# Optimization experiments

Hardware: AMD Instinct MI355X
Metric: run time of the kernel (lower is better)

The kernel has to match this reference:

```python
import jax, jax.numpy as jnp
import numpy as np
import itertools

B, H, W, C = 64, 28, 28, 576
NH, WS = 18, 7
KD = C // NH          # head dim = 32 (attn_ratio=1 so d == key_dim)
HID = 4 * C           # mlp hidden
N = WS * WS           # tokens per window = 49


def _bias_idxs():
    points = list(itertools.product(range(WS), range(WS)))
    offsets, idxs = {}, []
    for p1 in points:
        for p2 in points:
            off = (abs(p1[0] - p2[0]), abs(p1[1] - p2[1]))
            if off not in offsets:
                offsets[off] = len(offsets)
            idxs.append(offsets[off])
    return np.asarray(idxs, dtype=np.int64).reshape(N, N), len(offsets)


def setup_inputs() -> dict:
    key = jax.random.key(0)
    ks = jax.random.split(key, 10)
    idxs, n_off = _bias_idxs()  # n_off == 49
    s = 0.02
    return {
        "x": jax.random.normal(ks[0], (B, H * W, C), jnp.float32),
        "gamma_a": jnp.ones((C,), jnp.float32),
        "beta_a": jnp.zeros((C,), jnp.float32),
        "qkv_w": jax.random.normal(ks[1], (3 * C, C), jnp.float32) * s,
        "qkv_b": jnp.zeros((3 * C,), jnp.float32),
        "proj_w": jax.random.normal(ks[2], (C, C), jnp.float32) * s,
        "proj_b": jnp.zeros((C,), jnp.float32),
        "attn_biases": jax.random.normal(ks[3], (NH, n_off), jnp.float32) * s,
        "conv_w": jax.random.normal(ks[4], (C, 1, 3, 3), jnp.float32) * 0.1,
        "bn_gamma": jnp.ones((C,), jnp.float32),
        "bn_beta": jnp.zeros((C,), jnp.float32),
        "bn_mean": jnp.zeros((C,), jnp.float32),
        "bn_var": jax.random.uniform(ks[5], (C,), jnp.float32, 0.5, 1.5),
        "gamma_m": jnp.ones((C,), jnp.float32),
        "beta_m": jnp.zeros((C,), jnp.float32),
        "fc1_w": jax.random.normal(ks[6], (HID, C), jnp.float32) * s,
        "fc1_b": jnp.zeros((HID,), jnp.float32),
        "fc2_w": jax.random.normal(ks[7], (C, HID), jnp.float32) * s,
        "fc2_b": jnp.zeros((C,), jnp.float32),
        "bias_idxs": jnp.asarray(idxs),
    }


def _ln(x, g, b, eps=1e-5):
    mu = x.mean(-1, keepdims=True)
    var = ((x - mu) ** 2).mean(-1, keepdims=True)
    return (x - mu) * jax.lax.rsqrt(var + eps) * g + b


def reference(x, gamma_a, beta_a, qkv_w, qkv_b, proj_w, proj_b, attn_biases,
              conv_w, bn_gamma, bn_beta, bn_mean, bn_var,
              gamma_m, beta_m, fc1_w, fc1_b, fc2_w, fc2_b, bias_idxs):
    scale = KD ** -0.5
    nWh, nWw = H // WS, W // WS
    res = x
    # ---- window partition: (B, H*W, C) -> (B*nWh*nWw, 49, C) ----
    xw = x.reshape(B, nWh, WS, nWw, WS, C).transpose(0, 1, 3, 2, 4, 5)
    xw = xw.reshape(-1, N, C)
    # ---- windowed attention with gathered relative-position bias ----
    h = _ln(xw, gamma_a, beta_a)
    qkv = h @ qkv_w.T + qkv_b                       # (Bw, N, 3C)
    qkv = qkv.reshape(-1, N, NH, 3 * KD)
    q, k, v = jnp.split(qkv, 3, axis=-1)            # each (Bw, N, NH, KD)
    q = q.transpose(0, 2, 1, 3)
    k = k.transpose(0, 2, 1, 3)
    v = v.transpose(0, 2, 1, 3)
    bias = attn_biases[:, bias_idxs]                # (NH, N, N)
    attn = jnp.einsum('bhnd,bhmd->bhnm', q, k) * scale + bias
    attn = jax.nn.softmax(attn, axis=-1)
    out = jnp.einsum('bhnm,bhmd->bhnd', attn, v)    # (Bw, NH, N, KD)
    out = out.transpose(0, 2, 1, 3).reshape(-1, N, C) @ proj_w.T + proj_b
    # ---- window reverse ----
    out = out.reshape(B, nWh, nWw, WS, WS, C).transpose(0, 1, 3, 2, 4, 5)
    out = out.reshape(B, H * W, C)
    x = res + out
    # ---- depthwise 3x3 conv + BatchNorm (inference stats) ----
    xc = x.transpose(0, 2, 1).reshape(B, C, H, W)
    xc = jax.lax.conv_general_dilated(
        xc, conv_w, (1, 1), [(1, 1), (1, 1)],
        feature_group_count=C,
        dimension_numbers=('NCHW', 'OIHW', 'NCHW'))
    eps = 1e-5
    inv = (jax.lax.rsqrt(bn_var + eps) * bn_gamma)[:, None, None]
    xc = (xc - bn_mean[:, None, None]) * inv + bn_beta[:, None, None]
    x = xc.reshape(B, C, H * W).transpose(0, 2, 1)
    # ---- MLP with pre-LayerNorm ----
    hm = _ln(x, gamma_m, beta_m)
    hm = jax.nn.gelu(hm @ fc1_w.T + fc1_b, approximate=False)
    hm = hm @ fc2_w.T + fc2_b
    return x + hm
```

## Files before the change

kernel.cpp:

```cpp
#include <hip/hip_runtime.h>
#include <hip/hip_bf16.h>

typedef __bf16 v8bf  __attribute__((ext_vector_type(8)));
typedef __bf16 v4bf  __attribute__((ext_vector_type(4)));
typedef float  f32x4 __attribute__((ext_vector_type(4)));
typedef float  f32x8 __attribute__((ext_vector_type(8)));

#define TOKENS 50176
#define CDIM   576
#define NHEAD  18
#define QKVD   1728

__device__ __forceinline__ void gld16(const __bf16* g, __bf16* l)
{
    __builtin_amdgcn_global_load_lds(
        (const __attribute__((address_space(1))) void*)g,
        (__attribute__((address_space(3))) void*)l,
        16, 0, 0);
}

__device__ __forceinline__ float fast_gelu(float x)
{
    const float z  = x * 0.70710678118654752f;
    const float az = fabsf(z);
    const float t  = __frcp_rn(1.0f + 0.3275911f * az);
    float p = 1.061405429f;
    p = p * t - 1.453152027f;
    p = p * t + 1.421413741f;
    p = p * t - 0.284496736f;
    p = p * t + 0.254829592f;
    const float e   = __expf(-z * z);
    float erfv = 1.0f - p * t * e;
    erfv = copysignf(erfv, z);
    return 0.5f * x * (1.0f + erfv);
}

__global__ __launch_bounds__(256)
void cast4_kernel(const float* __restrict__ s0, const float* __restrict__ s1,
                  const float* __restrict__ s2, const float* __restrict__ s3,
                  __bf16* __restrict__ dst)
{
    const size_t i = ((size_t)blockIdx.x * 256 + threadIdx.x) * 4;
    constexpr size_t n0 = (size_t)QKVD * CDIM;
    constexpr size_t n1 = n0 + (size_t)CDIM * CDIM;
    constexpr size_t n2 = n1 + (size_t)2304 * CDIM;
    const float* s; size_t off;
    if (i < n0)      { s = s0; off = i; }
    else if (i < n1) { s = s1; off = i - n0; }
    else if (i < n2) { s = s2; off = i - n1; }
    else             { s = s3; off = i - n2; }
    f32x4 v = *(const f32x4*)&s[off];
    v4bf o;
#pragma unroll
    for (int j = 0; j < 4; ++j) o[j] = (__bf16)v[j];
    *(v4bf*)&dst[i] = o;
}

__global__ __launch_bounds__(64)
void conv_prep(const float* __restrict__ w, const float* __restrict__ bg,
               const float* __restrict__ bb, const float* __restrict__ bm,
               const float* __restrict__ bv, __bf16* __restrict__ wt,
               float* __restrict__ bias2)
{
    const int c = blockIdx.x * 64 + threadIdx.x;
    const float inv = rsqrtf(bv[c] + 1e-5f) * bg[c];
#pragma unroll
    for (int t = 0; t < 9; ++t) wt[t * CDIM + c] = (__bf16)(w[c * 9 + t] * inv);
    bias2[c] = bb[c] - bm[c] * inv;
}

__global__ __launch_bounds__(256)
void ln_kernel(const float* __restrict__ x, const float* __restrict__ g,
               const float* __restrict__ b, __bf16* __restrict__ out)
{
    const int lane = threadIdx.x & 63;
    const int wid  = threadIdx.x >> 6;
    const size_t t = (size_t)blockIdx.x * 4 + wid;
    const float* row = x + t * CDIM;

    float v[16];
    float sum = 0.f, sq = 0.f;
    {
        f32x8 d0 = *(const f32x8*)&row[(size_t)lane * 8];
#pragma unroll
        for (int j = 0; j < 8; ++j) { float f = d0[j]; v[j] = f; sum += f; sq += f * f; }
    }
    if (lane < 8) {
        f32x8 d1 = *(const f32x8*)&row[(size_t)(lane + 64) * 8];
#pragma unroll
        for (int j = 0; j < 8; ++j) { float f = d1[j]; v[8 + j] = f; sum += f; sq += f * f; }
    }
#pragma unroll
    for (int o = 32; o >= 1; o >>= 1) {
        sum += __shfl_xor(sum, o, 64);
        sq  += __shfl_xor(sq,  o, 64);
    }
    const float mean = sum * (1.0f / CDIM);
    const float rstd = rsqrtf(sq * (1.0f / CDIM) - mean * mean + 1e-5f);

    {
        int c0 = lane * 8;
        v8bf o0;
#pragma unroll
        for (int j = 0; j < 8; ++j)
            o0[j] = (__bf16)((v[j] - mean) * rstd * g[c0 + j] + b[c0 + j]);
        *(v8bf*)&out[t * CDIM + c0] = o0;
    }
    if (lane < 8) {
        int c0 = (lane + 64) * 8;
        v8bf o1;
#pragma unroll
        for (int j = 0; j < 8; ++j)
            o1[j] = (__bf16)((v[8 + j] - mean) * rstd * g[c0 + j] + b[c0 + j]);
        *(v8bf*)&out[t * CDIM + c0] = o1;
    }
}

template<int EPI, typename OutT, typename AddT>
__global__ __launch_bounds__(512, 1)
void gemm_bt(const __bf16* __restrict__ A, const __bf16* __restrict__ W,
             const float* __restrict__ bias, const AddT* __restrict__ add,
             OutT* __restrict__ C, int N, int K, int nN)
{
    constexpr int BK  = 32;
    constexpr int ASZ = 256 * BK;
    constexpr int BSZ = 192 * BK;
    __shared__ __bf16 L[4][ASZ + BSZ];
    const int tid = threadIdx.x, lane = tid & 63, wid = tid >> 6;
    const int lr = lane & 15, kh = lane >> 4;
    const int wm = wid >> 2, wn = wid & 3;

    const int nwg = gridDim.x, bid = blockIdx.x;
    const int q = nwg >> 3, r = nwg & 7;
    const int xcd = bid & 7, jc = bid >> 3;
    const int wgid = (xcd < r ? xcd * (q + 1) : r * (q + 1) + (xcd - r) * q) + jc;
    const int mblk = wgid / nN, nblk = wgid - mblk * nN;
    const int m0 = mblk * 256, n0 = nblk * 192;

    const __bf16* pA = A + (size_t)(m0 + wid * 32 + lr) * K + kh * 8;
    const __bf16* pW = W + (size_t)(n0 + (wid < 6 ? wid : 0) * 32 + lr) * K + kh * 8;

    auto stageA = [&](int s, int kt) {
#pragma unroll
        for (int i = 0; i < 2; ++i)
            gld16(pA + (size_t)(i * 16) * K + kt * BK, &L[s][(wid * 2 + i) * 512]);
    };
    auto stageB = [&](int s, int kt) {
        if (wid < 6) {
#pragma unroll
            for (int i = 0; i < 2; ++i)
                gld16(pW + (size_t)(i * 16) * K + kt * BK,
                      &L[s][ASZ + (wid * 2 + i) * 512]);
        }
    };

    const int lo = lane * 8;

    f32x4 acc[8][3] = {};
    const int NT = K / BK;

    stageA(0, 0); stageB(0, 0);
    stageA(1, 1); stageB(1, 1);

    for (int t = 0; t < NT; ++t) {
        if (t + 1 < NT) {
            if (wid < 6) asm volatile("s_waitcnt vmcnt(4)" ::: "memory");
            else         asm volatile("s_waitcnt vmcnt(2)" ::: "memory");
        } else {
            asm volatile("s_waitcnt vmcnt(0)" ::: "memory");
        }
        __builtin_amdgcn_s_barrier();

        const __bf16* Ls = L[t & 3];
        v8bf bfr[3], afr[4];

#pragma unroll
        for (int nf = 0; nf < 3; ++nf)
            bfr[nf] = *(const v8bf*)&Ls[ASZ + (wn * 3 + nf) * 512 + lo];
#pragma unroll
        for (int mf = 0; mf < 4; ++mf)
            afr[mf] = *(const v8bf*)&Ls[(wm * 8 + mf) * 512 + lo];

        if (t + 2 < NT) stageA((t + 2) & 3, t + 2);

        __builtin_amdgcn_s_setprio(1);
#pragma unroll
        for (int mf = 0; mf < 4; ++mf)
#pragma unroll
            for (int nf = 0; nf < 3; ++nf)
                acc[mf][nf] = __builtin_amdgcn_mfma_f32_16x16x32_bf16(
                    afr[mf], bfr[nf], acc[mf][nf], 0, 0, 0);
        __builtin_amdgcn_s_setprio(0);
        __builtin_amdgcn_s_barrier();

#pragma unroll
        for (int mf = 0; mf < 4; ++mf)
            afr[mf] = *(const v8bf*)&Ls[(wm * 8 + 4 + mf) * 512 + lo];

        if (t + 2 < NT) stageB((t + 2) & 3, t + 2);

        __builtin_amdgcn_s_setprio(1);
#pragma unroll
        for (int mf = 0; mf < 4; ++mf)
#pragma unroll
            for (int nf = 0; nf < 3; ++nf)
                acc[4 + mf][nf] = __builtin_amdgcn_mfma_f32_16x16x32_bf16(
                    afr[mf], bfr[nf], acc[4 + mf][nf], 0, 0, 0);
        __builtin_amdgcn_s_setprio(0);
    }

#pragma unroll
    for (int mf = 0; mf < 8; ++mf)
#pragma unroll
        for (int nf = 0; nf < 3; ++nf)
#pragma unroll
            for (int rr = 0; rr < 4; ++rr) {
                int row = m0 + wm * 128 + mf * 16 + kh * 4 + rr;
                int col = n0 + wn * 48 + nf * 16 + lr;
                float vv = acc[mf][nf][rr] + bias[col];
                if (EPI == 1) vv += (float)add[(size_t)row * N + col];
                if (EPI == 2) vv = fast_gelu(vv);
                C[(size_t)row * N + col] = (OutT)vv;
            }
}

__global__ __launch_bounds__(64)
void attn_kernel(const __bf16* __restrict__ qkv, const float* __restrict__ biases,
                 const int* __restrict__ bidx, __bf16* __restrict__ out)
{
    const int head = blockIdx.x;
    const int win  = blockIdx.y;
    const int tid  = threadIdx.x;
    const int b  = win >> 4;
    const int wy = (win >> 2) & 3;
    const int wx = win & 3;
    __shared__ float kk[49][32];
    __shared__ float vv[49][32];
    const size_t hb = (size_t)head * 96;

    for (int e = tid; e < 196; e += 64) {
        const int n = e >> 2, j = e & 3;
        const int iy = n / 7, ix = n - iy * 7;
        const size_t t = (size_t)b * 784 + (size_t)(wy * 7 + iy) * 28 + wx * 7 + ix;
        const __bf16* p = qkv + t * QKVD + hb;
        v8bf k8 = *(const v8bf*)&p[32 + j * 8];
        v8bf v8 = *(const v8bf*)&p[64 + j * 8];
        f32x4 k0, k1, v0, v1;
#pragma unroll
        for (int r = 0; r < 4; ++r) {
            k0[r] = (float)k8[r]; k1[r] = (float)k8[4 + r];
            v0[r] = (float)v8[r]; v1[r] = (float)v8[4 + r];
        }
        *(f32x4*)&kk[n][j * 8]     = k0;
        *(f32x4*)&kk[n][j * 8 + 4] = k1;
        *(f32x4*)&vv[n][j * 8]     = v0;
        *(f32x4*)&vv[n][j * 8 + 4] = v1;
    }
    f32x4 qv[8];
    size_t tmine = 0;
    if (tid < 49) {
        const int iy = tid / 7, ix = tid - iy * 7;
        tmine = (size_t)b * 784 + (size_t)(wy * 7 + iy) * 28 + wx * 7 + ix;
        const __bf16* p = qkv + tmine * QKVD + hb;
#pragma unroll
        for (int jj = 0; jj < 4; ++jj) {
            v8bf q8 = *(const v8bf*)&p[jj * 8];
#pragma unroll
            for (int r = 0; r < 4; ++r) {
                qv[2 * jj][r]     = (float)q8[r];
                qv[2 * jj + 1][r] = (float)q8[4 + r];
            }
        }
    }
    __syncthreads();
    if (tid >= 49) return;

    const float scale = 0.17677669529663687f;
    float s[49];
    float mx = -1e30f;
    const int*   brow = bidx + tid * 49;
    const float* bh   = biases + head * 49;
#pragma unroll
    for (int m = 0; m < 49; ++m) {
        const f32x4* krow = (const f32x4*)&kk[m][0];
        f32x4 d4 = {0.f, 0.f, 0.f, 0.f};
#pragma unroll
        for (int j = 0; j < 8; ++j) d4 += qv[j] * krow[j];
        float val = (d4[0] + d4[1] + d4[2] + d4[3]) * scale + bh[brow[m]];
        s[m] = val;
        mx = fmaxf(mx, val);
    }
    float sum = 0.f;
#pragma unroll
    for (int m = 0; m < 49; ++m) { float e = __expf(s[m] - mx); s[m] = e; sum += e; }
    const float rs = 1.0f / sum;

    f32x4 av[8] = {};
#pragma unroll
    for (int m = 0; m < 49; ++m) {
        const float sm = s[m];
        const f32x4* vrow = (const f32x4*)&vv[m][0];
#pragma unroll
        for (int j = 0; j < 8; ++j) av[j] += sm * vrow[j];
    }

    __bf16* op = out + tmine * CDIM + (size_t)head * 32;
#pragma unroll
    for (int jj = 0; jj < 4; ++jj) {
        v8bf o;
#pragma unroll
        for (int r = 0; r < 4; ++r) {
            o[r]     = (__bf16)(av[2 * jj][r] * rs);
            o[4 + r] = (__bf16)(av[2 * jj + 1][r] * rs);
        }
        *(v8bf*)&op[jj * 8] = o;
    }
}

__global__ __launch_bounds__(256)
void conv_bn_ln(const __bf16* __restrict__ xin, const __bf16* __restrict__ wt,
                const float* __restrict__ bias2, const float* __restrict__ g,
                const float* __restrict__ b,
                __bf16* __restrict__ x3, __bf16* __restrict__ lnm)
{
    const int lane = threadIdx.x & 63;
    const int wid  = threadIdx.x >> 6;
    const size_t p = (size_t)blockIdx.x * 4 + wid;
    const int bimg = (int)(p / 784);
    const int pix  = (int)(p - (size_t)bimg * 784);
    const int y = pix / 28, xx = pix - y * 28;
    const size_t rowbase = (size_t)bimg * 784;

    float v[16];
    float sum = 0.f, sq = 0.f;

    {
        const int c0 = lane * 8;
        float a[8];
        f32x4 b0 = *(const f32x4*)&bias2[c0];
        f32x4 b1 = *(const f32x4*)&bias2[c0 + 4];
#pragma unroll
        for (int j = 0; j < 4; ++j) { a[j] = b0[j]; a[4 + j] = b1[j]; }
#pragma unroll
        for (int dy = 0; dy < 3; ++dy) {
            int ny = y + dy - 1;
            if (ny < 0 || ny >= 28) continue;
#pragma unroll
            for (int dx = 0; dx < 3; ++dx) {
                int nx = xx + dx - 1;
                if (nx < 0 || nx >= 28) continue;
                v8bf xv = *(const v8bf*)&xin[(rowbase + ny * 28 + nx) * CDIM + c0];
                v8bf wv = *(const v8bf*)&wt[(dy * 3 + dx) * CDIM + c0];
#pragma unroll
                for (int j = 0; j < 8; ++j) a[j] += (float)xv[j] * (float)wv[j];
            }
        }
#pragma unroll
        for (int j = 0; j < 8; ++j) { v[j] = a[j]; sum += a[j]; sq += a[j] * a[j]; }
    }
    if (lane < 8) {
        const int c0 = 512 + lane * 8;
        float a[8];
        f32x4 b0 = *(const f32x4*)&bias2[c0];
        f32x4 b1 = *(const f32x4*)&bias2[c0 + 4];
#pragma unroll
        for (int j = 0; j < 4; ++j) { a[j] = b0[j]; a[4 + j] = b1[j]; }
#pragma unroll
        for (int dy = 0; dy < 3; ++dy) {
            int ny = y + dy - 1;
            if (ny < 0 || ny >= 28) continue;
#pragma unroll
            for (int dx = 0; dx < 3; ++dx) {
                int nx = xx + dx - 1;
                if (nx < 0 || nx >= 28) continue;
                v8bf xv = *(const v8bf*)&xin[(rowbase + ny * 28 + nx) * CDIM + c0];
                v8bf wv = *(const v8bf*)&wt[(dy * 3 + dx) * CDIM + c0];
#pragma unroll
                for (int j = 0; j < 8; ++j) a[j] += (float)xv[j] * (float)wv[j];
            }
        }
#pragma unroll
        for (int j = 0; j < 8; ++j) { v[8 + j] = a[j]; sum += a[j]; sq += a[j] * a[j]; }
    }

#pragma unroll
    for (int o = 32; o >= 1; o >>= 1) {
        sum += __shfl_xor(sum, o, 64);
        sq  += __shfl_xor(sq,  o, 64);
    }
    const float mean = sum * (1.0f / CDIM);
    const float rstd = rsqrtf(sq * (1.0f / CDIM) - mean * mean + 1e-5f);

    {
        const int c0 = lane * 8;
        v8bf o3, ol;
#pragma unroll
        for (int j = 0; j < 8; ++j) {
            o3[j] = (__bf16)v[j];
            ol[j] = (__bf16)((v[j] - mean) * rstd * g[c0 + j] + b[c0 + j]);
        }
        *(v8bf*)&x3[p * CDIM + c0]  = o3;
        *(v8bf*)&lnm[p * CDIM + c0] = ol;
    }
    if (lane < 8) {
        const int c0 = 512 + lane * 8;
        v8bf o3, ol;
#pragma unroll
        for (int j = 0; j < 8; ++j) {
            o3[j] = (__bf16)v[8 + j];
            ol[j] = (__bf16)((v[8 + j] - mean) * rstd * g[c0 + j] + b[c0 + j]);
        }
        *(v8bf*)&x3[p * CDIM + c0]  = o3;
        *(v8bf*)&lnm[p * CDIM + c0] = ol;
    }
}

extern "C" void kernel_launch(void* const* d_in, const int* in_sizes, int n_in,
                              void* d_out, int out_size, void* d_ws, size_t ws_size,
                              hipStream_t stream)
{
    (void)in_sizes; (void)n_in; (void)out_size; (void)ws_size;
    const float* x          = (const float*)d_in[0];
    const float* gamma_a    = (const float*)d_in[1];
    const float* beta_a     = (const float*)d_in[2];
    const float* qkv_w      = (const float*)d_in[3];
    const float* qkv_b      = (const float*)d_in[4];
    const float* proj_w     = (const float*)d_in[5];
    const float* proj_b     = (const float*)d_in[6];
    const float* attn_bias  = (const float*)d_in[7];
    const float* conv_w     = (const float*)d_in[8];
    const float* bn_g       = (const float*)d_in[9];
    const float* bn_b       = (const float*)d_in[10];
    const float* bn_m       = (const float*)d_in[11];
    const float* bn_v       = (const float*)d_in[12];
    const float* gamma_m    = (const float*)d_in[13];
    const float* beta_m     = (const float*)d_in[14];
    const float* fc1_w      = (const float*)d_in[15];
    const float* fc1_b      = (const float*)d_in[16];
    const float* fc2_w      = (const float*)d_in[17];
    const float* fc2_b      = (const float*)d_in[18];
    const int*   bidx       = (const int*)d_in[19];

    const size_t T = TOKENS;
    __bf16* ws     = (__bf16*)d_ws;
    __bf16* hbuf   = ws;
    __bf16* qkvbuf = ws + T * 576;
    __bf16* aout   = ws;
    __bf16* x2     = ws + T * 2304;
    __bf16* x3     = ws + T * 2880;
    __bf16* lnm    = ws;
    __bf16* f1     = ws + T * 576;
    __bf16* wq     = x3 + T * 576;
    __bf16* wp     = wq + (size_t)QKVD * CDIM;
    __bf16* w1     = wp + (size_t)CDIM * CDIM;
    __bf16* w2     = w1 + (size_t)2304 * CDIM;
    __bf16* wt     = w2 + (size_t)CDIM * 2304;
    float*  bias2  = (float*)(wt + 9 * CDIM);
    float*  outp   = (float*)d_out;

    cast4_kernel<<<dim3(3888), 256, 0, stream>>>(qkv_w, proj_w, fc1_w, fc2_w, wq);
    conv_prep<<<dim3(9), 64, 0, stream>>>(conv_w, bn_g, bn_b, bn_m, bn_v, wt, bias2);

    ln_kernel<<<dim3(T / 4), 256, 0, stream>>>(x, gamma_a, beta_a, hbuf);
    gemm_bt<0, __bf16, float><<<dim3(196 * 9), 512, 0, stream>>>(
        hbuf, wq, qkv_b, nullptr, qkvbuf, QKVD, CDIM, 9);
    attn_kernel<<<dim3(NHEAD, 1024), 64, 0, stream>>>(qkvbuf, attn_bias, bidx, aout);
    gemm_bt<1, __bf16, float><<<dim3(196 * 3), 512, 0, stream>>>(
        aout, wp, proj_b, x, x2, CDIM, CDIM, 3);
    conv_bn_ln<<<dim3(12544), 256, 0, stream>>>(x2, wt, bias2, gamma_m, beta_m,
                                                x3, lnm);
    gemm_bt<2, __bf16, float><<<dim3(196 * 12), 512, 0, stream>>>(
        lnm, w1, fc1_b, nullptr, f1, 2304, CDIM, 12);
    gemm_bt<1, float, __bf16><<<dim3(196 * 3), 512, 0, stream>>>(
        f1, w2, fc2_b, x3, outp, CDIM, 2304, 3);
}
```

Baseline: 1.003 ms.

## Switch GEMM to BK=64 double-buffered pipeline with one barrier per tile

Doubles the K tile to 64 and replaces the 4-stage, two-half-step pipeline with a 2-buffer scheme that prefetches the next tile after reading fragments. Each iteration waits for all outstanding loads, takes one barrier and runs 48 MFMAs per wave instead of 24. This halves loop iterations and barriers, but removes the deeper prefetch and the partial vmcnt waits, so load latency may be less hidden.

```diff
diff --git a/kernel.cpp b/kernel.cpp
--- a/kernel.cpp
+++ b/kernel.cpp
@@ -122,10 +122,10 @@
              const float* __restrict__ bias, const AddT* __restrict__ add,
              OutT* __restrict__ C, int N, int K, int nN)
 {
-    constexpr int BK  = 32;
+    constexpr int BK  = 64;
     constexpr int ASZ = 256 * BK;
     constexpr int BSZ = 192 * BK;
-    __shared__ __bf16 L[4][ASZ + BSZ];
+    __shared__ __bf16 L[2][ASZ + BSZ];
     const int tid = threadIdx.x, lane = tid & 63, wid = tid >> 6;
     const int lr = lane & 15, kh = lane >> 4;
     const int wm = wid >> 2, wn = wid & 3;
@@ -140,17 +140,20 @@
     const __bf16* pA = A + (size_t)(m0 + wid * 32 + lr) * K + kh * 8;
     const __bf16* pW = W + (size_t)(n0 + (wid < 6 ? wid : 0) * 32 + lr) * K + kh * 8;
 
-    auto stageA = [&](int s, int kt) {
-#pragma unroll
-        for (int i = 0; i < 2; ++i)
-            gld16(pA + (size_t)(i * 16) * K + kt * BK, &L[s][(wid * 2 + i) * 512]);
-    };
-    auto stageB = [&](int s, int kt) {
+    auto stage = [&](int s, int kt) {
+#pragma unroll
+        for (int h = 0; h < 2; ++h)
+#pragma unroll
+            for (int i = 0; i < 2; ++i)
+                gld16(pA + (size_t)(i * 16) * K + kt * BK + h * 32,
+                      &L[s][(h * 16 + wid * 2 + i) * 512]);
         if (wid < 6) {
 #pragma unroll
-            for (int i = 0; i < 2; ++i)
-                gld16(pW + (size_t)(i * 16) * K + kt * BK,
-                      &L[s][ASZ + (wid * 2 + i) * 512]);
+            for (int h = 0; h < 2; ++h)
+#pragma unroll
+                for (int i = 0; i < 2; ++i)
+                    gld16(pW + (size_t)(i * 16) * K + kt * BK + h * 32,
+                          &L[s][ASZ + (h * 12 + wid * 2 + i) * 512]);
         }
     };
 
@@ -159,53 +162,47 @@
     f32x4 acc[8][3] = {};
     const int NT = K / BK;
 
-    stageA(0, 0); stageB(0, 0);
-    stageA(1, 1); stageB(1, 1);
+    stage(0, 0);
 
     for (int t = 0; t < NT; ++t) {
-        if (t + 1 < NT) {
-            if (wid < 6) asm volatile("s_waitcnt vmcnt(4)" ::: "memory");
-            else         asm volatile("s_waitcnt vmcnt(2)" ::: "memory");
-        } else {
-            asm volatile("s_waitcnt vmcnt(0)" ::: "memory");
-        }
+        asm volatile("s_waitcnt vmcnt(0)" ::: "memory");
         __builtin_amdgcn_s_barrier();
 
-        const __bf16* Ls = L[t & 3];
-        v8bf bfr[3], afr[4];
+        const __bf16* Ls = L[t & 1];
+        v8bf bfr[3], afr[8];
 
 #pragma unroll
         for (int nf = 0; nf < 3; ++nf)
             bfr[nf] = *(const v8bf*)&Ls[ASZ + (wn * 3 + nf) * 512 + lo];
 #pragma unroll
-        for (int mf = 0; mf < 4; ++mf)
+        for (int mf = 0; mf < 8; ++mf)
             afr[mf] = *(const v8bf*)&Ls[(wm * 8 + mf) * 512 + lo];
 
-        if (t + 2 < NT) stageA((t + 2) & 3, t + 2);
+        if (t + 1 < NT) stage((t + 1) & 1, t + 1);
 
         __builtin_amdgcn_s_setprio(1);
 #pragma unroll
-        for (int mf = 0; mf < 4; ++mf)
+        for (int mf = 0; mf < 8; ++mf)
 #pragma unroll
             for (int nf = 0; nf < 3; ++nf)
                 acc[mf][nf] = __builtin_amdgcn_mfma_f32_16x16x32_bf16(
                     afr[mf], bfr[nf], acc[mf][nf], 0, 0, 0);
         __builtin_amdgcn_s_setprio(0);
-        __builtin_amdgcn_s_barrier();
-
-#pragma unroll
-        for (int mf = 0; mf < 4; ++mf)
-            afr[mf] = *(const v8bf*)&Ls[(wm * 8 + 4 + mf) * 512 + lo];
-
-        if (t + 2 < NT) stageB((t + 2) & 3, t + 2);
+
+#pragma unroll
+        for (int nf = 0; nf < 3; ++nf)
+            bfr[nf] = *(const v8bf*)&Ls[ASZ + (12 + wn * 3 + nf) * 512 + lo];
+#pragma unroll
+        for (int mf = 0; mf < 8; ++mf)
+            afr[mf] = *(const v8bf*)&Ls[(16 + wm * 8 + mf) * 512 + lo];
 
         __builtin_amdgcn_s_setprio(1);
 #pragma unroll
-        for (int mf = 0; mf < 4; ++mf)
+        for (int mf = 0; mf < 8; ++mf)
 #pragma unroll
             for (int nf = 0; nf < 3; ++nf)
-                acc[4 + mf][nf] = __builtin_amdgcn_mfma_f32_16x16x32_bf16(
-                    afr[mf], bfr[nf], acc[4 + mf][nf], 0, 0, 0);
+                acc[mf][nf] = __builtin_amdgcn_mfma_f32_16x16x32_bf16(
+                    afr[mf], bfr[nf], acc[mf][nf], 0, 0, 0);
         __builtin_amdgcn_s_setprio(0);
     }
 
```

Result: slower. 1.112 ms (+10.9%).

## Shrink GEMM tile to 128x192 with 4 waves and two blocks per CU

Applied to the files above, without the earlier changes.

The GEMM kernel moves from a 256x192 tile with 8 waves and one block per CU to a 128x192 tile with 4 waves and launch bounds allowing two blocks per CU. The LDS ring drops from four stages to three, and the B-tile staging is redistributed so every wave loads three rows. Grid sizes double to match. The aim is better latency hiding and less tail imbalance through more resident workgroups. The cost is lower per-block data reuse, since each B tile is now reloaded for half as many rows.

```diff
diff --git a/kernel.cpp b/kernel.cpp
--- a/kernel.cpp
+++ b/kernel.cpp
@@ -117,28 +117,28 @@
 }
 
 template<int EPI, typename OutT, typename AddT>
-__global__ __launch_bounds__(512, 1)
-void gemm_bt(const __bf16* __restrict__ A, const __bf16* __restrict__ W,
-             const float* __restrict__ bias, const AddT* __restrict__ add,
-             OutT* __restrict__ C, int N, int K, int nN)
+__global__ __launch_bounds__(256, 2)
+void gemm_bt2(const __bf16* __restrict__ A, const __bf16* __restrict__ W,
+              const float* __restrict__ bias, const AddT* __restrict__ add,
+              OutT* __restrict__ C, int N, int K, int nN)
 {
     constexpr int BK  = 32;
-    constexpr int ASZ = 256 * BK;
+    constexpr int ASZ = 128 * BK;
     constexpr int BSZ = 192 * BK;
-    __shared__ __bf16 L[4][ASZ + BSZ];
+    __shared__ __bf16 L[3][ASZ + BSZ];
     const int tid = threadIdx.x, lane = tid & 63, wid = tid >> 6;
     const int lr = lane & 15, kh = lane >> 4;
-    const int wm = wid >> 2, wn = wid & 3;
+    const int wn = wid;
 
     const int nwg = gridDim.x, bid = blockIdx.x;
     const int q = nwg >> 3, r = nwg & 7;
     const int xcd = bid & 7, jc = bid >> 3;
     const int wgid = (xcd < r ? xcd * (q + 1) : r * (q + 1) + (xcd - r) * q) + jc;
     const int mblk = wgid / nN, nblk = wgid - mblk * nN;
-    const int m0 = mblk * 256, n0 = nblk * 192;
+    const int m0 = mblk * 128, n0 = nblk * 192;
 
     const __bf16* pA = A + (size_t)(m0 + wid * 32 + lr) * K + kh * 8;
-    const __bf16* pW = W + (size_t)(n0 + (wid < 6 ? wid : 0) * 32 + lr) * K + kh * 8;
+    const __bf16* pW = W + (size_t)(n0 + wid * 48 + lr) * K + kh * 8;
 
     auto stageA = [&](int s, int kt) {
 #pragma unroll
@@ -146,12 +146,10 @@
             gld16(pA + (size_t)(i * 16) * K + kt * BK, &L[s][(wid * 2 + i) * 512]);
     };
     auto stageB = [&](int s, int kt) {
-        if (wid < 6) {
-#pragma unroll
-            for (int i = 0; i < 2; ++i)
-                gld16(pW + (size_t)(i * 16) * K + kt * BK,
-                      &L[s][ASZ + (wid * 2 + i) * 512]);
-        }
+#pragma unroll
+        for (int i = 0; i < 3; ++i)
+            gld16(pW + (size_t)(i * 16) * K + kt * BK,
+                  &L[s][ASZ + (wid * 3 + i) * 512]);
     };
 
     const int lo = lane * 8;
@@ -163,15 +161,11 @@
     stageA(1, 1); stageB(1, 1);
 
     for (int t = 0; t < NT; ++t) {
-        if (t + 1 < NT) {
-            if (wid < 6) asm volatile("s_waitcnt vmcnt(4)" ::: "memory");
-            else         asm volatile("s_waitcnt vmcnt(2)" ::: "memory");
-        } else {
-            asm volatile("s_waitcnt vmcnt(0)" ::: "memory");
-        }
+        if (t + 1 < NT) asm volatile("s_waitcnt vmcnt(5)" ::: "memory");
+        else            asm volatile("s_waitcnt vmcnt(0)" ::: "memory");
         __builtin_amdgcn_s_barrier();
 
-        const __bf16* Ls = L[t & 3];
+        const __bf16* Ls = L[t % 3];
         v8bf bfr[3], afr[4];
 
 #pragma unroll
@@ -179,9 +173,9 @@
             bfr[nf] = *(const v8bf*)&Ls[ASZ + (wn * 3 + nf) * 512 + lo];
 #pragma unroll
         for (int mf = 0; mf < 4; ++mf)
-            afr[mf] = *(const v8bf*)&Ls[(wm * 8 + mf) * 512 + lo];
-
-        if (t + 2 < NT) stageA((t + 2) & 3, t + 2);
+            afr[mf] = *(const v8bf*)&Ls[mf * 512 + lo];
+
+        if (t + 2 < NT) stageA((t + 2) % 3, t + 2);
 
         __builtin_amdgcn_s_setprio(1);
 #pragma unroll
@@ -195,9 +189,9 @@
 
 #pragma unroll
         for (int mf = 0; mf < 4; ++mf)
-            afr[mf] = *(const v8bf*)&Ls[(wm * 8 + 4 + mf) * 512 + lo];
-
-        if (t + 2 < NT) stageB((t + 2) & 3, t + 2);
+            afr[mf] = *(const v8bf*)&Ls[(4 + mf) * 512 + lo];
+
+        if (t + 2 < NT) stageB((t + 2) % 3, t + 2);
 
         __builtin_amdgcn_s_setprio(1);
 #pragma unroll
@@ -215,7 +209,7 @@
         for (int nf = 0; nf < 3; ++nf)
 #pragma unroll
             for (int rr = 0; rr < 4; ++rr) {
-                int row = m0 + wm * 128 + mf * 16 + kh * 4 + rr;
+                int row = m0 + mf * 16 + kh * 4 + rr;
                 int col = n0 + wn * 48 + nf * 16 + lr;
                 float vv = acc[mf][nf][rr] + bias[col];
                 if (EPI == 1) vv += (float)add[(size_t)row * N + col];
@@ -462,15 +456,15 @@
     conv_prep<<<dim3(9), 64, 0, stream>>>(conv_w, bn_g, bn_b, bn_m, bn_v, wt, bias2);
 
     ln_kernel<<<dim3(T / 4), 256, 0, stream>>>(x, gamma_a, beta_a, hbuf);
-    gemm_bt<0, __bf16, float><<<dim3(196 * 9), 512, 0, stream>>>(
+    gemm_bt2<0, __bf16, float><<<dim3(392 * 9), 256, 0, stream>>>(
         hbuf, wq, qkv_b, nullptr, qkvbuf, QKVD, CDIM, 9);
     attn_kernel<<<dim3(NHEAD, 1024), 64, 0, stream>>>(qkvbuf, attn_bias, bidx, aout);
-    gemm_bt<1, __bf16, float><<<dim3(196 * 3), 512, 0, stream>>>(
+    gemm_bt2<1, __bf16, float><<<dim3(392 * 3), 256, 0, stream>>>(
         aout, wp, proj_b, x, x2, CDIM, CDIM, 3);
     conv_bn_ln<<<dim3(12544), 256, 0, stream>>>(x2, wt, bias2, gamma_m, beta_m,
                                                 x3, lnm);
-    gemm_bt<2, __bf16, float><<<dim3(196 * 12), 512, 0, stream>>>(
+    gemm_bt2<2, __bf16, float><<<dim3(392 * 12), 256, 0, stream>>>(
         lnm, w1, fc1_b, nullptr, f1, 2304, CDIM, 12);
-    gemm_bt<1, float, __bf16><<<dim3(196 * 3), 512, 0, stream>>>(
+    gemm_bt2<1, float, __bf16><<<dim3(392 * 3), 256, 0, stream>>>(
         f1, w2, fc2_b, x3, outp, CDIM, 2304, 3);
 }
```

Result: no change. 1.022 ms (+1.9%).
